# Performance work log

Measured on AMD Instinct MI355X. Metric: run time of the kernel, lower is better.

Reference implementation:

```python
import jax, jax.numpy as jnp
import numpy as np


def _build_resonance(T):
    """res[i,j] = Omega(gcd(i+1, j+1)) = sum_p min(v_p(i+1), v_p(j+1))."""
    n = np.arange(1, T + 1)
    g = np.gcd.outer(n, n)  # [T,T], values in 1..T
    # smallest-prime-factor sieve up to T, then Omega (prime factors w/ multiplicity)
    spf = np.arange(T + 1)
    for i in range(2, int(T ** 0.5) + 1):
        if spf[i] == i:
            sl = spf[i * i:: i]
            np.minimum(sl, i, out=sl)
    omega = np.zeros(T + 1, np.int64)
    for m in range(2, T + 1):
        omega[m] = omega[m // spf[m]] + 1
    return omega[g].astype(np.float32)


def _build_buffers(T):
    res = _build_resonance(T)
    causal = np.tril(np.ones((T, T), np.float32))
    ident = np.eye(T, dtype=np.float32)
    allowed = ((res > 0) | (ident > 0)) & (causal > 0)  # bool [T,T]
    rbias = np.log1p(res) * allowed.astype(np.float32)
    return jnp.asarray(rbias), jnp.asarray(allowed)


def setup_inputs() -> dict:
    key = jax.random.key(0)
    B, T, C, H = 8, 2048, 1024, 64
    kx, kq, kk, kv = jax.random.split(key, 4)
    x = jax.random.normal(kx, (B, T, C), dtype=jnp.float32)
    scale = C ** -0.5
    Wq = jax.random.normal(kq, (C, H), dtype=jnp.float32) * scale
    Wk = jax.random.normal(kk, (C, H), dtype=jnp.float32) * scale
    Wv = jax.random.normal(kv, (C, H), dtype=jnp.float32) * scale
    rbias, allowed = _build_buffers(T)
    return {"x": x, "Wq": Wq, "Wk": Wk, "Wv": Wv, "rbias": rbias, "allowed": allowed}


def reference(x, Wq, Wk, Wv, rbias, allowed):
    B, T, C = x.shape
    q = x @ Wq  # [B,T,H]
    k = x @ Wk
    v = x @ Wv
    w = jnp.einsum("bth,bsh->bts", q, k) * (C ** -0.5)  # note: scaled by C, as in source
    w = w + rbias[:T, :T]
    w = jnp.where(allowed[:T, :T], w, -jnp.inf)
    a = jax.nn.softmax(w, axis=-1)  # every row has diagonal allowed -> no NaN
    return a @ v  # [B,T,H]
```

## Files before the change

kernel.cpp:

```cpp
#include <hip/hip_runtime.h>

#define T_SEQ 2048
#define NB    8
#define CDIM  1024
#define HDIM  64
#define PPB   80

typedef __attribute__((ext_vector_type(8))) short short8;
typedef __attribute__((ext_vector_type(4))) short short4v;
typedef __attribute__((ext_vector_type(4))) float float4v;

__device__ inline short f2bf(float x) {
    unsigned u = __builtin_bit_cast(unsigned int, x);
    u += 0x7FFFu + ((u >> 16) & 1u);
    return (short)(u >> 16);
}

__device__ inline void dma16(const void* g, void* l) {
    __builtin_amdgcn_global_load_lds(
        (const __attribute__((address_space(1))) unsigned int*)g,
        (__attribute__((address_space(3))) unsigned int*)l, 16, 0, 0);
}

template<int CTRL> __device__ inline float dppf(float v) {
    return __builtin_bit_cast(float,
        __builtin_amdgcn_update_dpp(0, __builtin_bit_cast(int, v), CTRL, 0xF, 0xF, true));
}
__device__ inline float rowmax16(float v) {
    v = fmaxf(v, dppf<0xB1>(v));  v = fmaxf(v, dppf<0x4E>(v));
    v = fmaxf(v, dppf<0x141>(v)); v = fmaxf(v, dppf<0x140>(v));
    return v;
}
__device__ inline float rowsum16(float v) {
    v += dppf<0xB1>(v);  v += dppf<0x4E>(v);
    v += dppf<0x141>(v); v += dppf<0x140>(v);
    return v;
}

__global__ __launch_bounds__(256) void wcvt_kernel(
    const float* __restrict__ Wq, const float* __restrict__ Wk,
    const float* __restrict__ Wv, short* __restrict__ Wbt)
{
    __shared__ float tile[64][65];
    const int w  = blockIdx.y;
    const int k0 = blockIdx.x * 64;
    const float* Ws[3] = {Wq, Wk, Wv};
    const float* W = Ws[w];
    const int n  = threadIdx.x & 63;
    const int kq = threadIdx.x >> 6;
#pragma unroll
    for (int i = 0; i < 16; ++i) {
        int kk = kq + i * 4;
        tile[kk][n] = W[(size_t)(k0 + kk) * HDIM + n];
    }
    __syncthreads();
    const int kk = threadIdx.x & 63;
#pragma unroll
    for (int i = 0; i < 16; ++i) {
        int nn = kq + i * 4;
        Wbt[((size_t)(w * HDIM + nn)) * CDIM + k0 + kk] = f2bf(tile[kk][nn]);
    }
}

__global__ __launch_bounds__(512) void proj_kernel(
    const float* __restrict__ x, const short* __restrict__ Wbt,
    short* __restrict__ qb, short* __restrict__ kb, short* __restrict__ vtb)
{
    __shared__ short As[2][32 * 64];
    __shared__ short Bs[2][192 * 64];

    const int tid  = threadIdx.x;
    const int wave = tid >> 6, lane = tid & 63;
    const int quad = lane >> 4, l16 = lane & 15;
    const int mt   = wave >> 2;
    const int cg   = wave & 3;
    const int m0   = blockIdx.x * 32;

    const int arow = tid >> 4;
    const int ac   = tid & 15;
    const int asw  = (((ac >> 1) ^ (arow & 7)) * 8) + (ac & 1) * 4;
    const float* xsrc = x + (size_t)(m0 + arow) * CDIM + ac * 4;

    const int brow = tid >> 3;
    const int bsw  = ((tid & 7) ^ (brow & 7)) * 8;

    float4v acc[3];
#pragma unroll
    for (int i = 0; i < 3; ++i) acc[i] = (float4v){0.f, 0.f, 0.f, 0.f};

    {
        float4 a = *(const float4*)xsrc;
#pragma unroll
        for (int i = 0; i < 3; ++i)
            dma16(Wbt + (size_t)(i * 64 + brow) * CDIM + bsw,
                  &Bs[0][i * 4096 + tid * 8]);
        short4v s; s[0]=f2bf(a.x); s[1]=f2bf(a.y); s[2]=f2bf(a.z); s[3]=f2bf(a.w);
        *(short4v*)&As[0][arow * 64 + asw] = s;
    }

    int p = 0;
    for (int kt = 0; kt < 16; ++kt) {
        __syncthreads();
        const bool more = (kt + 1) < 16;
        float4 a;
        if (more) {
            a = *(const float4*)(xsrc + (kt + 1) * 64);
#pragma unroll
            for (int i = 0; i < 3; ++i)
                dma16(Wbt + (size_t)(i * 64 + brow) * CDIM + (kt + 1) * 64 + bsw,
                      &Bs[p ^ 1][i * 4096 + tid * 8]);
        }
#pragma unroll
        for (int ks = 0; ks < 2; ++ks) {
            const int cs = ((ks * 4 + quad) ^ (l16 & 7)) * 8;
            short8 af = *(const short8*)&As[p][(mt * 16 + l16) * 64 + cs];
#pragma unroll
            for (int i = 0; i < 3; ++i) {
                const int ct = cg * 3 + i;
                short8 bf_ = *(const short8*)&Bs[p][(ct * 16 + l16) * 64 + cs];
                acc[i] = __builtin_amdgcn_mfma_f32_16x16x32_bf16(af, bf_, acc[i], 0, 0, 0);
            }
        }
        if (more) {
            short4v s; s[0]=f2bf(a.x); s[1]=f2bf(a.y); s[2]=f2bf(a.z); s[3]=f2bf(a.w);
            *(short4v*)&As[p ^ 1][arow * 64 + asw] = s;
        }
        p ^= 1;
    }

#pragma unroll
    for (int i = 0; i < 3; ++i) {
        const int ctg = cg * 3 + i;
        const int mat = ctg >> 2;
        const int n   = (ctg & 3) * 16 + l16;
#pragma unroll
        for (int r = 0; r < 4; ++r) {
            const int m = m0 + mt * 16 + quad * 4 + r;
            if (mat == 0)      qb[(size_t)m * HDIM + n] = f2bf(acc[i][r] * 0.03125f);
            else if (mat == 1) kb[(size_t)m * HDIM + n] = f2bf(acc[i][r]);
            else {
                int bb = m >> 11, tt = m & (T_SEQ - 1);
                vtb[((size_t)bb * HDIM + n) * T_SEQ + tt] = f2bf(acc[i][r]);
            }
        }
    }
}

__global__ __launch_bounds__(256) void attn_part_kernel(
    const short* __restrict__ qb, const short* __restrict__ kb,
    const short* __restrict__ vtb, const float* __restrict__ rbias,
    float* __restrict__ Op, float2* __restrict__ mlp)
{
    __shared__ short Ks[2][64 * 64];
    __shared__ short Vs[2][64 * 64];
    __shared__ short Ps[4][16][72];

    const int b   = blockIdx.y;
    const int tid = threadIdx.x;
    const int wave = tid >> 6, lane = tid & 63;
    const int quad = lane >> 4, l16 = lane & 15;
    const int swz  = l16 & 7;
    const int srow = tid >> 3;
    const int gchk = ((tid & 7) ^ (srow & 7)) * 8;

    const int bx = (int)(gridDim.x - 1 - blockIdx.x);
    int qt64 = 0, c = bx, cum = 0;
    while (true) { int ch = (qt64 + 8) >> 3; if (c < ch) break; c -= ch; cum += ch; ++qt64; }
    const int j0 = c * 8;
    const int j1 = (j0 + 8 < qt64 + 1) ? j0 + 8 : qt64 + 1;
    const int qrow0 = qt64 * 64 + wave * 16;

    const short* qptr = qb + (size_t)(b * T_SEQ + qrow0 + l16) * HDIM;
    short8 qf0 = *(const short8*)(qptr + quad * 8);
    short8 qf1 = *(const short8*)(qptr + 32 + quad * 8);

    float4v oacc[4];
#pragma unroll
    for (int i = 0; i < 4; ++i) oacc[i] = (float4v){0.f, 0.f, 0.f, 0.f};
    float m_run[4] = {-1e30f, -1e30f, -1e30f, -1e30f};
    float l_run[4] = {0.f, 0.f, 0.f, 0.f};

    {
        const int s0 = j0 * 64;
#pragma unroll
        for (int i = 0; i < 2; ++i) {
            dma16(kb + (size_t)(b * T_SEQ + s0 + i * 32 + srow) * HDIM + gchk,
                  &Ks[0][i * 2048 + tid * 8]);
            dma16(vtb + (size_t)(b * HDIM + i * 32 + srow) * T_SEQ + s0 + gchk,
                  &Vs[0][i * 2048 + tid * 8]);
        }
    }

    int p = 0;
    for (int j = j0; j < j1; ++j) {
        __syncthreads();
        const int s0 = j * 64;

        float rbv[4][4];
#pragma unroll
        for (int nt = 0; nt < 4; ++nt) {
            int s_idx = s0 + nt * 16 + l16;
#pragma unroll
            for (int r = 0; r < 4; ++r)
                rbv[nt][r] = rbias[(size_t)(qrow0 + quad * 4 + r) * T_SEQ + s_idx];
        }

        if (j + 1 < j1) {
            const int sn = (j + 1) * 64;
#pragma unroll
            for (int i = 0; i < 2; ++i) {
                dma16(kb + (size_t)(b * T_SEQ + sn + i * 32 + srow) * HDIM + gchk,
                      &Ks[p ^ 1][i * 2048 + tid * 8]);
                dma16(vtb + (size_t)(b * HDIM + i * 32 + srow) * T_SEQ + sn + gchk,
                      &Vs[p ^ 1][i * 2048 + tid * 8]);
            }
        }

        float4v sa[4];
#pragma unroll
        for (int nt = 0; nt < 4; ++nt) {
            const int rbase = (nt * 16 + l16) * 64;
            short8 kf0 = *(const short8*)&Ks[p][rbase + ((quad ^ swz) * 8)];
            short8 kf1 = *(const short8*)&Ks[p][rbase + (((4 + quad) ^ swz) * 8)];
            float4v a = {0.f, 0.f, 0.f, 0.f};
            a = __builtin_amdgcn_mfma_f32_16x16x32_bf16(qf0, kf0, a, 0, 0, 0);
            a = __builtin_amdgcn_mfma_f32_16x16x32_bf16(qf1, kf1, a, 0, 0, 0);
            sa[nt] = a;
        }

        float pm[4][4];
        float mt[4] = {-1e30f, -1e30f, -1e30f, -1e30f};
#pragma unroll
        for (int nt = 0; nt < 4; ++nt) {
            int s_idx = s0 + nt * 16 + l16;
#pragma unroll
            for (int r = 0; r < 4; ++r) {
                int t_idx = qrow0 + quad * 4 + r;
                float rb = rbv[nt][r];
                bool ok = (rb > 0.f) || ((t_idx == 0) && (s_idx == 0));
                float sv = ok ? (sa[nt][r] + rb) : -1e30f;
                pm[nt][r] = sv;
                mt[r] = fmaxf(mt[r], sv);
            }
        }
        float alpha[4];
#pragma unroll
        for (int r = 0; r < 4; ++r) {
            float mn = fmaxf(m_run[r], rowmax16(mt[r]));
            alpha[r] = __expf(m_run[r] - mn);
            m_run[r] = mn;
        }
        float rs[4] = {0.f, 0.f, 0.f, 0.f};
#pragma unroll
        for (int nt = 0; nt < 4; ++nt)
#pragma unroll
            for (int r = 0; r < 4; ++r) {
                float pv = (pm[nt][r] > -1e29f) ? __expf(pm[nt][r] - m_run[r]) : 0.f;
                pm[nt][r] = pv;
                rs[r] += pv;
            }
#pragma unroll
        for (int r = 0; r < 4; ++r) {
            l_run[r] = l_run[r] * alpha[r] + rowsum16(rs[r]);
            oacc[0][r] *= alpha[r]; oacc[1][r] *= alpha[r];
            oacc[2][r] *= alpha[r]; oacc[3][r] *= alpha[r];
        }

#pragma unroll
        for (int nt = 0; nt < 4; ++nt)
#pragma unroll
            for (int r = 0; r < 4; ++r)
                Ps[wave][quad * 4 + r][nt * 16 + l16] = f2bf(pm[nt][r]);

#pragma unroll
        for (int ks = 0; ks < 2; ++ks) {
            short8 pf = *(const short8*)&Ps[wave][l16][ks * 32 + quad * 8];
#pragma unroll
            for (int ht = 0; ht < 4; ++ht) {
                short8 vf = *(const short8*)&Vs[p][(ht * 16 + l16) * 64
                            + (((ks * 4 + quad) ^ swz) * 8)];
                oacc[ht] = __builtin_amdgcn_mfma_f32_16x16x32_bf16(pf, vf, oacc[ht], 0, 0, 0);
            }
        }
        p ^= 1;
    }

    const int pidx = b * PPB + cum + c;
    float* obase = Op + (size_t)pidx * 4096;
#pragma unroll
    for (int ht = 0; ht < 4; ++ht)
#pragma unroll
        for (int r = 0; r < 4; ++r)
            obase[(wave * 16 + quad * 4 + r) * 64 + ht * 16 + l16] = oacc[ht][r];
    if (l16 == 0)
#pragma unroll
        for (int r = 0; r < 4; ++r)
            mlp[(size_t)pidx * 64 + wave * 16 + quad * 4 + r] = make_float2(m_run[r], l_run[r]);
}

__global__ __launch_bounds__(256) void attn_merge_kernel(
    const float* __restrict__ Op, const float2* __restrict__ mlp,
    float* __restrict__ out)
{
    const int qt16 = blockIdx.x;
    const int b    = blockIdx.y;
    const int qt64 = qt16 >> 2;
    const int nch  = (qt64 + 8) >> 3;
    const int g8   = qt64 >> 3, rem = qt64 & 7;
    const int cum  = 4 * g8 * (g8 + 1) + rem * (g8 + 1);
    const int pbase = b * PPB + cum;

    const int row = threadIdx.x >> 4;
    const int c4  = (threadIdx.x & 15) * 4;
    const int prow = (qt16 & 3) * 16 + row;

    float2 ml[4];
    float4 o4[4];
#pragma unroll
    for (int cc = 0; cc < 4; ++cc) {
        ml[cc] = mlp[(size_t)(pbase + cc) * 64 + prow];
        o4[cc] = *(const float4*)&Op[(size_t)(pbase + cc) * 4096 + prow * 64 + c4];
        if (cc >= nch) ml[cc].x = -1e30f;
    }
    float M = -1e30f;
#pragma unroll
    for (int cc = 0; cc < 4; ++cc) M = fmaxf(M, ml[cc].x);
    float L = 0.f;
    float4 O = make_float4(0.f, 0.f, 0.f, 0.f);
#pragma unroll
    for (int cc = 0; cc < 4; ++cc) {
        float w = __expf(ml[cc].x - M);
        L += ml[cc].y * w;
        O.x += o4[cc].x * w; O.y += o4[cc].y * w;
        O.z += o4[cc].z * w; O.w += o4[cc].w * w;
    }
    float inv = 1.0f / L;
    float4 res = make_float4(O.x * inv, O.y * inv, O.z * inv, O.w * inv);
    *(float4*)&out[((size_t)(b * T_SEQ) + qt16 * 16 + row) * HDIM + c4] = res;
}

extern "C" void kernel_launch(void* const* d_in, const int* in_sizes, int n_in,
                              void* d_out, int out_size, void* d_ws, size_t ws_size,
                              hipStream_t stream) {
    (void)in_sizes; (void)n_in; (void)out_size; (void)ws_size;
    const float* x     = (const float*)d_in[0];
    const float* Wq    = (const float*)d_in[1];
    const float* Wk    = (const float*)d_in[2];
    const float* Wv    = (const float*)d_in[3];
    const float* rbias = (const float*)d_in[4];
    float* out = (float*)d_out;

    char* wsb   = (char*)d_ws;
    short* qb   = (short*)(wsb);
    short* kb   = (short*)(wsb + (size_t)2 * 1024 * 1024);
    short* vtb  = (short*)(wsb + (size_t)4 * 1024 * 1024);
    short* Wbt  = (short*)(wsb + (size_t)6 * 1024 * 1024);
    float* Op   = (float*)(wsb + (size_t)7 * 1024 * 1024);
    float2* mlp = (float2*)(wsb + (size_t)18 * 1024 * 1024);

    wcvt_kernel<<<dim3(16, 3), 256, 0, stream>>>(Wq, Wk, Wv, Wbt);
    proj_kernel<<<dim3(512), 512, 0, stream>>>(x, Wbt, qb, kb, vtb);
    attn_part_kernel<<<dim3(PPB, NB), 256, 0, stream>>>(qb, kb, vtb, rbias, Op, mlp);
    attn_merge_kernel<<<dim3(128, NB), 256, 0, stream>>>(Op, mlp, out);
}
```

Baseline: 170.4 us.

## Prepack causal bias to bf16 MFMA layout and fuse split-K merge into attention

A prep kernel now converts the fp32 rbias into a compact bf16 tile layout that matches the MFMA fragment order, with disallowed entries set to a large negative sentinel. Each attention wave then reads its bias with two vector loads instead of sixteen strided fp32 loads, and the mask test drops out of the inner loop. The separate merge kernel is removed: query tiles with a single chunk write the output directly, and the other chunks use an atomic counter so the last block merges the partials. This costs a memset, an extra bias pass that is repeated on every call, and bf16 rounding of the bias.

Measured after the change: 272.8 us. 1.6x slower.

```diff
diff --git a/kernel.cpp b/kernel.cpp
--- a/kernel.cpp
+++ b/kernel.cpp
@@ -15,6 +15,9 @@
     u += 0x7FFFu + ((u >> 16) & 1u);
     return (short)(u >> 16);
 }
+__device__ inline float bf2f(short v) {
+    return __builtin_bit_cast(float, ((unsigned)(unsigned short)v) << 16);
+}
 
 __device__ inline void dma16(const void* g, void* l) {
     __builtin_amdgcn_global_load_lds(
@@ -37,28 +40,57 @@
     return v;
 }
 
-__global__ __launch_bounds__(256) void wcvt_kernel(
+__global__ __launch_bounds__(256) void prep_kernel(
     const float* __restrict__ Wq, const float* __restrict__ Wk,
-    const float* __restrict__ Wv, short* __restrict__ Wbt)
+    const float* __restrict__ Wv, const float* __restrict__ rbias,
+    short* __restrict__ Wbt, short* __restrict__ biasPk)
 {
-    __shared__ float tile[64][65];
-    const int w  = blockIdx.y;
-    const int k0 = blockIdx.x * 64;
-    const float* Ws[3] = {Wq, Wk, Wv};
-    const float* W = Ws[w];
-    const int n  = threadIdx.x & 63;
-    const int kq = threadIdx.x >> 6;
-#pragma unroll
-    for (int i = 0; i < 16; ++i) {
-        int kk = kq + i * 4;
-        tile[kk][n] = W[(size_t)(k0 + kk) * HDIM + n];
-    }
-    __syncthreads();
-    const int kk = threadIdx.x & 63;
-#pragma unroll
-    for (int i = 0; i < 16; ++i) {
-        int nn = kq + i * 4;
-        Wbt[((size_t)(w * HDIM + nn)) * CDIM + k0 + kk] = f2bf(tile[kk][nn]);
+    const int qt16 = blockIdx.x;
+    const int tid  = threadIdx.x;
+    const int wave = tid >> 6, lane = tid & 63;
+    const int quad = lane >> 4, l16 = lane & 15;
+
+    if (blockIdx.y == 0 && qt16 < 48) {
+        __shared__ float tile[64][65];
+        const int w  = qt16 >> 4;
+        const int k0 = (qt16 & 15) * 64;
+        const float* Ws[3] = {Wq, Wk, Wv};
+        const float* W = Ws[w];
+        const int n  = tid & 63;
+        const int kq = tid >> 6;
+#pragma unroll
+        for (int i = 0; i < 16; ++i)
+            tile[kq + i * 4][n] = W[(size_t)(k0 + kq + i * 4) * HDIM + n];
+        __syncthreads();
+        const int kk = tid & 63;
+#pragma unroll
+        for (int i = 0; i < 16; ++i) {
+            int nn = kq + i * 4;
+            Wbt[((size_t)(w * HDIM + nn)) * CDIM + k0 + kk] = f2bf(tile[kk][nn]);
+        }
+    }
+
+    const int a  = qt16 >> 2;
+    const int jw = (int)blockIdx.y * 4 + wave;
+    if (jw <= a) {
+        const short SENT = f2bf(-1e38f);
+        short8 lo, hi;
+#pragma unroll
+        for (int nt = 0; nt < 4; ++nt) {
+            const int s = jw * 64 + nt * 16 + l16;
+#pragma unroll
+            for (int r = 0; r < 4; ++r) {
+                const int t = qt16 * 16 + quad * 4 + r;
+                float rb = rbias[(size_t)t * T_SEQ + s];
+                bool ok = (rb > 0.f) || ((t == 0) && (s == 0));
+                short v = ok ? f2bf(rb) : SENT;
+                if (nt < 2) lo[nt * 4 + r] = v; else hi[(nt - 2) * 4 + r] = v;
+            }
+        }
+        short* dst = biasPk + ((size_t)((2 * a + (qt16 & 3)) * (a + 1) + jw)) * 1024
+                   + lane * 16;
+        *(short8*)dst = lo;
+        *(short8*)(dst + 8) = hi;
     }
 }
 
@@ -146,14 +178,16 @@
     }
 }
 
-__global__ __launch_bounds__(256) void attn_part_kernel(
+__global__ __launch_bounds__(256) void attn_kernel(
     const short* __restrict__ qb, const short* __restrict__ kb,
-    const short* __restrict__ vtb, const float* __restrict__ rbias,
-    float* __restrict__ Op, float2* __restrict__ mlp)
+    const short* __restrict__ vtb, const short* __restrict__ biasPk,
+    float* __restrict__ Op, float2* __restrict__ mlp,
+    int* __restrict__ cnt, float* __restrict__ out)
 {
     __shared__ short Ks[2][64 * 64];
     __shared__ short Vs[2][64 * 64];
     __shared__ short Ps[4][16][72];
+    __shared__ int lastv;
 
     const int b   = blockIdx.y;
     const int tid = threadIdx.x;
@@ -169,6 +203,7 @@
     const int j0 = c * 8;
     const int j1 = (j0 + 8 < qt64 + 1) ? j0 + 8 : qt64 + 1;
     const int qrow0 = qt64 * 64 + wave * 16;
+    const size_t boff = (size_t)(2 * qt64 + wave) * (qt64 + 1);
 
     const short* qptr = qb + (size_t)(b * T_SEQ + qrow0 + l16) * HDIM;
     short8 qf0 = *(const short8*)(qptr + quad * 8);
@@ -194,16 +229,10 @@
     int p = 0;
     for (int j = j0; j < j1; ++j) {
         __syncthreads();
-        const int s0 = j * 64;
-
-        float rbv[4][4];
-#pragma unroll
-        for (int nt = 0; nt < 4; ++nt) {
-            int s_idx = s0 + nt * 16 + l16;
-#pragma unroll
-            for (int r = 0; r < 4; ++r)
-                rbv[nt][r] = rbias[(size_t)(qrow0 + quad * 4 + r) * T_SEQ + s_idx];
-        }
+
+        const short* bp = biasPk + (boff + j) * 1024 + lane * 16;
+        short8 bl0 = *(const short8*)bp;
+        short8 bl1 = *(const short8*)(bp + 8);
 
         if (j + 1 < j1) {
             const int sn = (j + 1) * 64;
@@ -222,27 +251,23 @@
             const int rbase = (nt * 16 + l16) * 64;
             short8 kf0 = *(const short8*)&Ks[p][rbase + ((quad ^ swz) * 8)];
             short8 kf1 = *(const short8*)&Ks[p][rbase + (((4 + quad) ^ swz) * 8)];
-            float4v a = {0.f, 0.f, 0.f, 0.f};
-            a = __builtin_amdgcn_mfma_f32_16x16x32_bf16(qf0, kf0, a, 0, 0, 0);
-            a = __builtin_amdgcn_mfma_f32_16x16x32_bf16(qf1, kf1, a, 0, 0, 0);
-            sa[nt] = a;
+            float4v acc_ = {0.f, 0.f, 0.f, 0.f};
+            acc_ = __builtin_amdgcn_mfma_f32_16x16x32_bf16(qf0, kf0, acc_, 0, 0, 0);
+            acc_ = __builtin_amdgcn_mfma_f32_16x16x32_bf16(qf1, kf1, acc_, 0, 0, 0);
+            sa[nt] = acc_;
         }
 
         float pm[4][4];
         float mt[4] = {-1e30f, -1e30f, -1e30f, -1e30f};
 #pragma unroll
-        for (int nt = 0; nt < 4; ++nt) {
-            int s_idx = s0 + nt * 16 + l16;
+        for (int nt = 0; nt < 4; ++nt)
 #pragma unroll
             for (int r = 0; r < 4; ++r) {
-                int t_idx = qrow0 + quad * 4 + r;
-                float rb = rbv[nt][r];
-                bool ok = (rb > 0.f) || ((t_idx == 0) && (s_idx == 0));
-                float sv = ok ? (sa[nt][r] + rb) : -1e30f;
+                short rv = (nt < 2) ? bl0[nt * 4 + r] : bl1[(nt - 2) * 4 + r];
+                float sv = sa[nt][r] + bf2f(rv);
                 pm[nt][r] = sv;
                 mt[r] = fmaxf(mt[r], sv);
             }
-        }
         float alpha[4];
 #pragma unroll
         for (int r = 0; r < 4; ++r) {
@@ -255,7 +280,7 @@
         for (int nt = 0; nt < 4; ++nt)
 #pragma unroll
             for (int r = 0; r < 4; ++r) {
-                float pv = (pm[nt][r] > -1e29f) ? __expf(pm[nt][r] - m_run[r]) : 0.f;
+                float pv = __expf(pm[nt][r] - m_run[r]);
                 pm[nt][r] = pv;
                 rs[r] += pv;
             }
@@ -285,7 +310,21 @@
         p ^= 1;
     }
 
-    const int pidx = b * PPB + cum + c;
+    const int nch = (qt64 + 8) >> 3;
+    if (nch == 1) {
+#pragma unroll
+        for (int r = 0; r < 4; ++r) {
+            float inv = 1.0f / l_run[r];
+            float* orow = out + (size_t)(b * T_SEQ + qrow0 + quad * 4 + r) * HDIM;
+#pragma unroll
+            for (int ht = 0; ht < 4; ++ht)
+                orow[ht * 16 + l16] = oacc[ht][r] * inv;
+        }
+        return;
+    }
+
+    const int pbase = b * PPB + cum;
+    const int pidx  = pbase + c;
     float* obase = Op + (size_t)pidx * 4096;
 #pragma unroll
     for (int ht = 0; ht < 4; ++ht)
@@ -296,47 +335,42 @@
 #pragma unroll
         for (int r = 0; r < 4; ++r)
             mlp[(size_t)pidx * 64 + wave * 16 + quad * 4 + r] = make_float2(m_run[r], l_run[r]);
-}
-
-__global__ __launch_bounds__(256) void attn_merge_kernel(
-    const float* __restrict__ Op, const float2* __restrict__ mlp,
-    float* __restrict__ out)
-{
-    const int qt16 = blockIdx.x;
-    const int b    = blockIdx.y;
-    const int qt64 = qt16 >> 2;
-    const int nch  = (qt64 + 8) >> 3;
-    const int g8   = qt64 >> 3, rem = qt64 & 7;
-    const int cum  = 4 * g8 * (g8 + 1) + rem * (g8 + 1);
-    const int pbase = b * PPB + cum;
-
-    const int row = threadIdx.x >> 4;
-    const int c4  = (threadIdx.x & 15) * 4;
-    const int prow = (qt16 & 3) * 16 + row;
-
+
+    __threadfence();
+    __syncthreads();
+    if (tid == 0) lastv = atomicAdd(&cnt[b * 32 + qt64], 1);
+    __syncthreads();
+    if (lastv != nch - 1) return;
+    __threadfence();
+
+    const int row = tid >> 2;
+    const int cg4 = tid & 3;
     float2 ml[4];
-    float4 o4[4];
 #pragma unroll
     for (int cc = 0; cc < 4; ++cc) {
-        ml[cc] = mlp[(size_t)(pbase + cc) * 64 + prow];
-        o4[cc] = *(const float4*)&Op[(size_t)(pbase + cc) * 4096 + prow * 64 + c4];
+        ml[cc] = mlp[(size_t)(pbase + cc) * 64 + row];
         if (cc >= nch) ml[cc].x = -1e30f;
     }
     float M = -1e30f;
 #pragma unroll
     for (int cc = 0; cc < 4; ++cc) M = fmaxf(M, ml[cc].x);
-    float L = 0.f;
-    float4 O = make_float4(0.f, 0.f, 0.f, 0.f);
-#pragma unroll
-    for (int cc = 0; cc < 4; ++cc) {
-        float w = __expf(ml[cc].x - M);
-        L += ml[cc].y * w;
-        O.x += o4[cc].x * w; O.y += o4[cc].y * w;
-        O.z += o4[cc].z * w; O.w += o4[cc].w * w;
-    }
-    float inv = 1.0f / L;
-    float4 res = make_float4(O.x * inv, O.y * inv, O.z * inv, O.w * inv);
-    *(float4*)&out[((size_t)(b * T_SEQ) + qt16 * 16 + row) * HDIM + c4] = res;
+    float wgt[4]; float L = 0.f;
+#pragma unroll
+    for (int cc = 0; cc < 4; ++cc) { wgt[cc] = __expf(ml[cc].x - M); L += ml[cc].y * wgt[cc]; }
+    const float inv = 1.0f / L;
+#pragma unroll
+    for (int pass = 0; pass < 4; ++pass) {
+        const int col = (cg4 + pass * 4) * 4;
+        float4 O = make_float4(0.f, 0.f, 0.f, 0.f);
+#pragma unroll
+        for (int cc = 0; cc < 4; ++cc) {
+            float4 o4 = *(const float4*)&Op[(size_t)(pbase + cc) * 4096 + row * 64 + col];
+            O.x += o4.x * wgt[cc]; O.y += o4.y * wgt[cc];
+            O.z += o4.z * wgt[cc]; O.w += o4.w * wgt[cc];
+        }
+        float4 res = make_float4(O.x * inv, O.y * inv, O.z * inv, O.w * inv);
+        *(float4*)&out[((size_t)(b * T_SEQ) + qt64 * 64 + row) * HDIM + col] = res;
+    }
 }
 
 extern "C" void kernel_launch(void* const* d_in, const int* in_sizes, int n_in,
@@ -350,16 +384,18 @@
     const float* rbias = (const float*)d_in[4];
     float* out = (float*)d_out;
 
-    char* wsb   = (char*)d_ws;
-    short* qb   = (short*)(wsb);
-    short* kb   = (short*)(wsb + (size_t)2 * 1024 * 1024);
-    short* vtb  = (short*)(wsb + (size_t)4 * 1024 * 1024);
-    short* Wbt  = (short*)(wsb + (size_t)6 * 1024 * 1024);
-    float* Op   = (float*)(wsb + (size_t)7 * 1024 * 1024);
-    float2* mlp = (float2*)(wsb + (size_t)18 * 1024 * 1024);
-
-    wcvt_kernel<<<dim3(16, 3), 256, 0, stream>>>(Wq, Wk, Wv, Wbt);
+    char* wsb     = (char*)d_ws;
+    short* qb     = (short*)(wsb);
+    short* kb     = (short*)(wsb + (size_t)2 * 1024 * 1024);
+    short* vtb    = (short*)(wsb + (size_t)4 * 1024 * 1024);
+    short* Wbt    = (short*)(wsb + (size_t)6 * 1024 * 1024);
+    int*   cnt    = (int*)(wsb + (size_t)6 * 1024 * 1024 + 512 * 1024);
+    short* biasPk = (short*)(wsb + (size_t)7 * 1024 * 1024);
+    float* Op     = (float*)(wsb + (size_t)12 * 1024 * 1024);
+    float2* mlp   = (float2*)(wsb + (size_t)23 * 1024 * 1024);
+
+    hipMemsetAsync(cnt, 0, NB * 32 * sizeof(int), stream);
+    prep_kernel<<<dim3(128, 8), 256, 0, stream>>>(Wq, Wk, Wv, rbias, Wbt, biasPk);
     proj_kernel<<<dim3(512), 512, 0, stream>>>(x, Wbt, qb, kb, vtb);
-    attn_part_kernel<<<dim3(PPB, NB), 256, 0, stream>>>(qb, kb, vtb, rbias, Op, mlp);
-    attn_merge_kernel<<<dim3(128, NB), 256, 0, stream>>>(Op, mlp, out);
-}
+    attn_kernel<<<dim3(PPB, NB), 256, 0, stream>>>(qb, kb, vtb, biasPk, Op, mlp, cnt, out);
+}
```
